# Kernel optimization log

Hardware: AMD Instinct MI355X
Metric: run time of the kernel (lower is better)

## Reference

```python
import jax, jax.numpy as jnp
import numpy as np

ALPHA = 3.0
NITERS = 15
POWER_ITERS = 20
ROOTS = [np.cos(np.pi * (2 * i + 1) / (2 * NITERS)) for i in range(NITERS)]


def batch_conv2d(inputs, kernels):
    # inputs: [B,1,H,W], kernels: [B,1,3,3]; per-sample 3x3 stencil via grouped conv
    B, _, H, W = inputs.shape
    out = jax.lax.conv_general_dilated(
        inputs.reshape(1, B, H, W), kernels,
        window_strides=(1, 1), padding=((1, 1), (1, 1)),
        feature_group_count=B,
        dimension_numbers=("NCHW", "OIHW", "NCHW"))
    return out.reshape(B, 1, H, W)


def setup_inputs() -> dict:
    key = jax.random.key(0)
    k1, k2, k3, k4 = jax.random.split(key, 4)
    B, H, W = 64, 512, 512
    x = jax.random.normal(k1, (B, 1, H, W), dtype=jnp.float32)
    f = jax.random.normal(k2, (B, 1, H, W), dtype=jnp.float32)
    kernelA = jax.random.normal(k3, (B, 1, 3, 3), dtype=jnp.float32)
    u = jax.random.normal(k4, (B, 1, H, W), dtype=jnp.float32)
    return {"x": x, "f": f, "kernelA": kernelA, "u": u}


def reference(x, f, kernelA, u):
    # Power iteration to estimate the dominant eigenvalue magnitude m per sample
    for _ in range(POWER_ITERS):
        y = batch_conv2d(u, kernelA)
        m = jnp.max(jnp.abs(y), axis=(2, 3), keepdims=True)  # [B,1,1,1]
        u = y / m
    # Chebyshev step sizes over the band [m/alpha, m]
    taus = jnp.stack(
        [2.0 / (m + m / ALPHA - (m / ALPHA - m) * r) for r in ROOTS])  # [niters,B,1,1,1]

    def cheby_step(xc, tau):
        Ax = batch_conv2d(xc, kernelA)
        return xc + tau * (f - Ax), None

    x, _ = jax.lax.scan(cheby_step, x, taus)
    return x
```

## Files before the change

### kernel.cpp

```cpp
#include <hip/hip_runtime.h>

#define BB 64
#define HH 512
#define WW 512
#define PLANE (HH * WW)
#define N_CHEBY 15
#define FD 5
#define RR 32
#define NS (HH / RR)
#define STEPS (RR + 2 * FD)

struct F8 { float v[8]; };

__device__ __forceinline__ float wshr1(float x) {
    return __int_as_float(__builtin_amdgcn_update_dpp(
        0, __float_as_int(x), 0x138, 0xF, 0xF, true));
}
__device__ __forceinline__ float wshl1(float x) {
    return __int_as_float(__builtin_amdgcn_update_dpp(
        0, __float_as_int(x), 0x130, 0xF, 0xF, true));
}

__device__ __forceinline__ F8 ldrow(const float* plane, int y, int lane, bool ok) {
    F8 r;
    if (ok) {
        const float4* p =
            reinterpret_cast<const float4*>(plane + (size_t)y * WW + (lane << 3));
        const float4 a = p[0], b = p[1];
        r.v[0] = a.x; r.v[1] = a.y; r.v[2] = a.z; r.v[3] = a.w;
        r.v[4] = b.x; r.v[5] = b.y; r.v[6] = b.z; r.v[7] = b.w;
    } else {
#pragma unroll
        for (int i = 0; i < 8; ++i) r.v[i] = 0.f;
    }
    return r;
}

__device__ __forceinline__ void racc8(const F8& r, float k0, float k1, float k2,
                                      float acc[8]) {
    const float lf = wshr1(r.v[7]);
    const float rt = wshl1(r.v[0]);
    acc[0] = fmaf(k0, lf, fmaf(k1, r.v[0], fmaf(k2, r.v[1], acc[0])));
#pragma unroll
    for (int c = 1; c < 7; ++c)
        acc[c] = fmaf(k0, r.v[c-1], fmaf(k1, r.v[c], fmaf(k2, r.v[c+1], acc[c])));
    acc[7] = fmaf(k0, r.v[6], fmaf(k1, r.v[7], fmaf(k2, rt, acc[7])));
}

__global__ __launch_bounds__(256, 1) void conv_wave(
    const float* __restrict__ in, const float* __restrict__ kern,
    const float* __restrict__ pm_prev, float* __restrict__ out,
    float* __restrict__ pmw, float* __restrict__ pmz)
{
    const int lane = threadIdx.x & 63;
    const int wid  = threadIdx.x >> 6;
    const int b = blockIdx.y;
    const int stripe = (blockIdx.x << 2) + wid;
    const int ytop = stripe * RR;

    float invv = 1.f;
    if (pm_prev) {
        float v = (lane < NS) ? pm_prev[b * NS + lane] : 0.f;
#pragma unroll
        for (int o = 32; o; o >>= 1) v = fmaxf(v, __shfl_xor(v, o, 64));
        invv = 1.f / v;
    }

    const float* kb = kern + b * 9;
    const float k00=kb[0],k01=kb[1],k02=kb[2],k10=kb[3],k11=kb[4],k12=kb[5],
                k20=kb[6],k21=kb[7],k22=kb[8];
    const float* ip = in + (size_t)b * PLANE;
    float* op = out ? out + (size_t)b * PLANE : nullptr;

    F8 u2 = {}, u1 = {};
    F8 lt[FD - 1] = {}, lm[FD - 1] = {};
    float mz = 0.f, mw = 0.f;
    F8 u0 = ldrow(ip, ytop - FD, lane, (unsigned)(ytop - FD) < HH);

#pragma unroll 6
    for (int p = 0; p < STEPS; ++p) {
        const int yL = ytop - FD + p;
        F8 un = ldrow(ip, yL + 1, lane,
                      (p < STEPS - 1) && ((unsigned)(yL + 1) < HH));

        F8 nw[FD - 1];
        {
            float acc[8] = {0,0,0,0,0,0,0,0};
            racc8(u2, k00,k01,k02, acc);
            racc8(u1, k10,k11,k12, acc);
            racc8(u0, k20,k21,k22, acc);
            const int y = yL - 1;
            const bool act = (y >= ytop - (FD-1)) && (y <= ytop + RR + FD - 2)
                          && ((unsigned)y < HH);
#pragma unroll
            for (int c = 0; c < 8; ++c) nw[0].v[c] = act ? acc[c] * invv : 0.f;
        }
#pragma unroll
        for (int j = 2; j <= FD; ++j) {
            float acc[8] = {0,0,0,0,0,0,0,0};
            racc8(lt[j-2], k00,k01,k02, acc);
            racc8(lm[j-2], k10,k11,k12, acc);
            racc8(nw[j-2], k20,k21,k22, acc);
            const int y = yL - j;
            if (j < FD) {
                const bool act = (y >= ytop - (FD-j)) && (y <= ytop + RR + FD - j - 1)
                              && ((unsigned)y < HH);
#pragma unroll
                for (int c = 0; c < 8; ++c) nw[j-1].v[c] = act ? acc[c] : 0.f;
                if (j == FD - 1) {
#pragma unroll
                    for (int c = 0; c < 8; ++c)
                        mz = fmaxf(mz, fabsf(nw[j-1].v[c]));
                }
            } else {
                if (y >= ytop && y < ytop + RR) {
#pragma unroll
                    for (int c = 0; c < 8; ++c) mw = fmaxf(mw, fabsf(acc[c]));
                    if (op) {
                        float4* q = reinterpret_cast<float4*>(
                            op + (size_t)y * WW + (lane << 3));
                        q[0] = make_float4(acc[0], acc[1], acc[2], acc[3]);
                        q[1] = make_float4(acc[4], acc[5], acc[6], acc[7]);
                    }
                }
            }
        }
#pragma unroll
        for (int l = 0; l < FD - 1; ++l) { lt[l] = lm[l]; lm[l] = nw[l]; }
        u2 = u1; u1 = u0; u0 = un;
    }

#pragma unroll
    for (int o = 32; o; o >>= 1) {
        mz = fmaxf(mz, __shfl_xor(mz, o, 64));
        mw = fmaxf(mw, __shfl_xor(mw, o, 64));
    }
    if (lane == 0) {
        pmz[b * NS + stripe] = mz;
        pmw[b * NS + stripe] = mw;
    }
}

__global__ __launch_bounds__(64) void tau_k(
    const float* __restrict__ pmz, const float* __restrict__ pmw,
    float* __restrict__ taus)
{
    const int b = blockIdx.x, t = threadIdx.x;
    float vz = (t < NS) ? pmz[b * NS + t] : 0.f;
    float vw = (t < NS) ? pmw[b * NS + t] : 0.f;
#pragma unroll
    for (int o = 32; o; o >>= 1) {
        vz = fmaxf(vz, __shfl_xor(vz, o, 64));
        vw = fmaxf(vw, __shfl_xor(vw, o, 64));
    }
    if (t < N_CHEBY) {
        const float m = vw / vz;
        const double rr = cos(M_PI * (2.0 * t + 1.0) / (2.0 * N_CHEBY));
        const float denom = m + m / 3.0f - (m / 3.0f - m) * (float)rr;
        taus[t * BB + b] = 2.0f / denom;
    }
}

template<int RRv>
__global__ __launch_bounds__(256, 2) void cheby_wave2(
    const float* __restrict__ xin, const float* __restrict__ fin,
    const float* __restrict__ kern, const float* __restrict__ tauv,
    float* __restrict__ xout)
{
    constexpr int NSv = HH / RRv;
    constexpr int STEPSv = RRv + 2 * FD;
    __shared__ float fring[4][FD + 1][8][64];
    const int lane = threadIdx.x & 63;
    const int wid  = threadIdx.x >> 6;
    const int b = blockIdx.y;
    const int stripe = (blockIdx.x << 2) + wid;
    const int ytop = stripe * RRv;
    float (*fr)[8][64] = fring[wid];

    const float* kb = kern + b * 9;
    const float k00=kb[0],k01=kb[1],k02=kb[2],k10=kb[3],k11=kb[4],k12=kb[5],
                k20=kb[6],k21=kb[7],k22=kb[8];
    float tau[FD];
#pragma unroll
    for (int j = 0; j < FD; ++j) tau[j] = tauv[j * BB + b];

    const float* xp = xin + (size_t)b * PLANE;
    const float* fp = fin + (size_t)b * PLANE;
    float* op = xout + (size_t)b * PLANE;

    F8 u2 = {}, u1 = {};
    F8 lt[FD - 1] = {}, lm[FD - 1] = {};
    F8 u0 = ldrow(xp, ytop - FD, lane, (unsigned)(ytop - FD) < HH);

#pragma unroll 2
    for (int p = 0; p < STEPSv; ++p) {
        const int yL = ytop - FD + p;
        F8 un = ldrow(xp, yL + 1, lane,
                      (p < STEPSv - 1) && ((unsigned)(yL + 1) < HH));
        F8 fn = ldrow(fp, yL, lane, (p < STEPSv - 1) && ((unsigned)yL < HH));

        F8 ft[FD];
#pragma unroll
        for (int j = 1; j <= FD; ++j) {
            const int sp = (p + (FD + 1) - j) % (FD + 1);
#pragma unroll
            for (int c = 0; c < 8; ++c) ft[j-1].v[c] = fr[sp][c][lane];
        }

        F8 nw[FD - 1];
        {
            float acc[8] = {0,0,0,0,0,0,0,0};
            racc8(u2, k00,k01,k02, acc);
            racc8(u1, k10,k11,k12, acc);
            racc8(u0, k20,k21,k22, acc);
            const int y = yL - 1;
            const bool act = (y >= ytop - (FD-1)) && (y <= ytop + RRv + FD - 2)
                          && ((unsigned)y < HH);
#pragma unroll
            for (int c = 0; c < 8; ++c)
                nw[0].v[c] = act ? fmaf(tau[0], ft[0].v[c] - acc[c], u1.v[c]) : 0.f;
        }
#pragma unroll
        for (int j = 2; j <= FD; ++j) {
            float acc[8] = {0,0,0,0,0,0,0,0};
            racc8(lt[j-2], k00,k01,k02, acc);
            racc8(lm[j-2], k10,k11,k12, acc);
            racc8(nw[j-2], k20,k21,k22, acc);
            const int y = yL - j;
            if (j < FD) {
                const bool act = (y >= ytop - (FD-j)) && (y <= ytop + RRv + FD - j - 1)
                              && ((unsigned)y < HH);
#pragma unroll
                for (int c = 0; c < 8; ++c)
                    nw[j-1].v[c] =
                        act ? fmaf(tau[j-1], ft[j-1].v[c] - acc[c], lm[j-2].v[c])
                            : 0.f;
            } else {
                if (y >= ytop && y < ytop + RRv) {
                    float4* q = reinterpret_cast<float4*>(
                        op + (size_t)y * WW + (lane << 3));
                    float o0 = fmaf(tau[FD-1], ft[FD-1].v[0] - acc[0], lm[j-2].v[0]);
                    float o1 = fmaf(tau[FD-1], ft[FD-1].v[1] - acc[1], lm[j-2].v[1]);
                    float o2 = fmaf(tau[FD-1], ft[FD-1].v[2] - acc[2], lm[j-2].v[2]);
                    float o3 = fmaf(tau[FD-1], ft[FD-1].v[3] - acc[3], lm[j-2].v[3]);
                    q[0] = make_float4(o0, o1, o2, o3);
                    o0 = fmaf(tau[FD-1], ft[FD-1].v[4] - acc[4], lm[j-2].v[4]);
                    o1 = fmaf(tau[FD-1], ft[FD-1].v[5] - acc[5], lm[j-2].v[5]);
                    o2 = fmaf(tau[FD-1], ft[FD-1].v[6] - acc[6], lm[j-2].v[6]);
                    o3 = fmaf(tau[FD-1], ft[FD-1].v[7] - acc[7], lm[j-2].v[7]);
                    q[1] = make_float4(o0, o1, o2, o3);
                }
            }
        }

        if (p < STEPSv - 1) {
            const int sp = p % (FD + 1);
#pragma unroll
            for (int c = 0; c < 8; ++c) fr[sp][c][lane] = fn.v[c];
        }

#pragma unroll
        for (int l = 0; l < FD - 1; ++l) { lt[l] = lm[l]; lm[l] = nw[l]; }
        u2 = u1; u1 = u0; u0 = un;
    }
}

extern "C" void kernel_launch(void* const* d_in, const int* in_sizes, int n_in,
                              void* d_out, int out_size, void* d_ws, size_t ws_size,
                              hipStream_t stream)
{
    const float* x_in = (const float*)d_in[0];
    const float* f_in = (const float*)d_in[1];
    const float* k_in = (const float*)d_in[2];
    const float* u_in = (const float*)d_in[3];
    float* out = (float*)d_out;

    float* bufA = (float*)d_ws;
    float* pmW0 = bufA + (size_t)BB * PLANE;
    float* pmW1 = pmW0 + BB * NS;
    float* pmZ  = pmW1 + BB * NS;
    float* taus = pmZ  + BB * NS;

    dim3 blk(256);
    dim3 grdc(NS / 4, BB);

    conv_wave<<<grdc, blk, 0, stream>>>(u_in, k_in, nullptr, bufA, pmW0, pmZ);
    conv_wave<<<grdc, blk, 0, stream>>>(bufA, k_in, pmW0, out,  pmW1, pmZ);
    conv_wave<<<grdc, blk, 0, stream>>>(out,  k_in, pmW1, bufA, pmW0, pmZ);
    conv_wave<<<grdc, blk, 0, stream>>>(bufA, k_in, pmW0, nullptr, pmW1, pmZ);

    tau_k<<<BB, 64, 0, stream>>>(pmZ, pmW1, taus);

    dim3 grdy((HH / 16) / 4, BB);
    cheby_wave2<16><<<grdy, blk, 0, stream>>>(x_in, f_in, k_in, taus,          out);
    cheby_wave2<16><<<grdy, blk, 0, stream>>>(out,  f_in, k_in, taus + 5 * BB, bufA);
    cheby_wave2<16><<<grdy, blk, 0, stream>>>(bufA, f_in, k_in, taus + 10 * BB, out);
}
```

Baseline: 343.2 us.

## Fuse more power iterations per conv launch, cutting four launches to three

Turns the power-iteration conv kernel into a template over the number of fused stencil steps. It then runs 7+7+6 steps in three launches instead of 5 steps in each of four launches. This removes one full-plane read/write round trip and one kernel launch. In exchange, each stripe carries a wider halo (more redundant rows of compute per 32-row stripe) and more registers of in-flight rows. The unroll factor is also reduced.

```diff
diff --git a/kernel.cpp b/kernel.cpp
--- a/kernel.cpp
+++ b/kernel.cpp
@@ -8,7 +8,6 @@
 #define FD 5
 #define RR 32
 #define NS (HH / RR)
-#define STEPS (RR + 2 * FD)
 
 struct F8 { float v[8]; };
 
@@ -47,11 +46,13 @@
     acc[7] = fmaf(k0, r.v[6], fmaf(k1, r.v[7], fmaf(k2, rt, acc[7])));
 }
 
-__global__ __launch_bounds__(256, 1) void conv_wave(
+template<int FDv>
+__global__ __launch_bounds__(256, 1) void conv_waveT(
     const float* __restrict__ in, const float* __restrict__ kern,
     const float* __restrict__ pm_prev, float* __restrict__ out,
     float* __restrict__ pmw, float* __restrict__ pmz)
 {
+    constexpr int STEPSv = RR + 2 * FDv;
     const int lane = threadIdx.x & 63;
     const int wid  = threadIdx.x >> 6;
     const int b = blockIdx.y;
@@ -73,41 +74,41 @@
     float* op = out ? out + (size_t)b * PLANE : nullptr;
 
     F8 u2 = {}, u1 = {};
-    F8 lt[FD - 1] = {}, lm[FD - 1] = {};
+    F8 lt[FDv - 1] = {}, lm[FDv - 1] = {};
     float mz = 0.f, mw = 0.f;
-    F8 u0 = ldrow(ip, ytop - FD, lane, (unsigned)(ytop - FD) < HH);
-
-#pragma unroll 6
-    for (int p = 0; p < STEPS; ++p) {
-        const int yL = ytop - FD + p;
+    F8 u0 = ldrow(ip, ytop - FDv, lane, (unsigned)(ytop - FDv) < HH);
+
+#pragma unroll 2
+    for (int p = 0; p < STEPSv; ++p) {
+        const int yL = ytop - FDv + p;
         F8 un = ldrow(ip, yL + 1, lane,
-                      (p < STEPS - 1) && ((unsigned)(yL + 1) < HH));
-
-        F8 nw[FD - 1];
+                      (p < STEPSv - 1) && ((unsigned)(yL + 1) < HH));
+
+        F8 nw[FDv - 1];
         {
             float acc[8] = {0,0,0,0,0,0,0,0};
             racc8(u2, k00,k01,k02, acc);
             racc8(u1, k10,k11,k12, acc);
             racc8(u0, k20,k21,k22, acc);
             const int y = yL - 1;
-            const bool act = (y >= ytop - (FD-1)) && (y <= ytop + RR + FD - 2)
+            const bool act = (y >= ytop - (FDv-1)) && (y <= ytop + RR + FDv - 2)
                           && ((unsigned)y < HH);
 #pragma unroll
             for (int c = 0; c < 8; ++c) nw[0].v[c] = act ? acc[c] * invv : 0.f;
         }
 #pragma unroll
-        for (int j = 2; j <= FD; ++j) {
+        for (int j = 2; j <= FDv; ++j) {
             float acc[8] = {0,0,0,0,0,0,0,0};
             racc8(lt[j-2], k00,k01,k02, acc);
             racc8(lm[j-2], k10,k11,k12, acc);
             racc8(nw[j-2], k20,k21,k22, acc);
             const int y = yL - j;
-            if (j < FD) {
-                const bool act = (y >= ytop - (FD-j)) && (y <= ytop + RR + FD - j - 1)
+            if (j < FDv) {
+                const bool act = (y >= ytop - (FDv-j)) && (y <= ytop + RR + FDv - j - 1)
                               && ((unsigned)y < HH);
 #pragma unroll
                 for (int c = 0; c < 8; ++c) nw[j-1].v[c] = act ? acc[c] : 0.f;
-                if (j == FD - 1) {
+                if (j == FDv - 1) {
 #pragma unroll
                     for (int c = 0; c < 8; ++c)
                         mz = fmaxf(mz, fabsf(nw[j-1].v[c]));
@@ -126,7 +127,7 @@
             }
         }
 #pragma unroll
-        for (int l = 0; l < FD - 1; ++l) { lt[l] = lm[l]; lm[l] = nw[l]; }
+        for (int l = 0; l < FDv - 1; ++l) { lt[l] = lm[l]; lm[l] = nw[l]; }
         u2 = u1; u1 = u0; u0 = un;
     }
 
@@ -167,7 +168,6 @@
     const float* __restrict__ kern, const float* __restrict__ tauv,
     float* __restrict__ xout)
 {
-    constexpr int NSv = HH / RRv;
     constexpr int STEPSv = RRv + 2 * FD;
     __shared__ float fring[4][FD + 1][8][64];
     const int lane = threadIdx.x & 63;
@@ -284,12 +284,11 @@
     dim3 blk(256);
     dim3 grdc(NS / 4, BB);
 
-    conv_wave<<<grdc, blk, 0, stream>>>(u_in, k_in, nullptr, bufA, pmW0, pmZ);
-    conv_wave<<<grdc, blk, 0, stream>>>(bufA, k_in, pmW0, out,  pmW1, pmZ);
-    conv_wave<<<grdc, blk, 0, stream>>>(out,  k_in, pmW1, bufA, pmW0, pmZ);
-    conv_wave<<<grdc, blk, 0, stream>>>(bufA, k_in, pmW0, nullptr, pmW1, pmZ);
-
-    tau_k<<<BB, 64, 0, stream>>>(pmZ, pmW1, taus);
+    conv_waveT<7><<<grdc, blk, 0, stream>>>(u_in, k_in, nullptr, bufA, pmW0, pmZ);
+    conv_waveT<7><<<grdc, blk, 0, stream>>>(bufA, k_in, pmW0, out,  pmW1, pmZ);
+    conv_waveT<6><<<grdc, blk, 0, stream>>>(out,  k_in, pmW1, nullptr, pmW0, pmZ);
+
+    tau_k<<<BB, 64, 0, stream>>>(pmZ, pmW0, taus);
 
     dim3 grdy((HH / 16) / 4, BB);
     cheby_wave2<16><<<grdy, blk, 0, stream>>>(x_in, f_in, k_in, taus,          out);
```

New measurement: 350.9 us. 2.2% more time.
